# Performance work log

Measured on AMD Instinct MI355X. Metric: run time of the kernel, lower is better.

Reference implementation:

```python
import jax, jax.numpy as jnp
from jax import lax
import numpy as np

N, C_IN, C_OUT, H, W, DS = 32, 16, 1, 128, 128, 5
NC = C_OUT * C_IN  # channels fed to DUBlock convs (= out_nc*nc_d[0])


def autocorr(x, ds):
    """x:(N,C,H,W) -> xtx_raw:(N,C,C,2ds-1,2ds-1).
    xtx_raw[n,i,j,u,v] = sum_{h,w} x[n,i,h,w] * xpad[n,j,u+h,v+w]  (zero pad ds-1),
    matching torch cal_xtx (sample-wise conv3d of x with itself)."""
    n, c, h, w = x.shape
    p = ds - 1
    xp = jnp.pad(x, ((0, 0), (0, 0), (p, p), (p, p)))
    rows = []
    for u in range(2 * ds - 1):
        cols = [jnp.einsum('nihw,njhw->nij', x,
                           lax.slice(xp, (0, 0, u, v), (n, c, u + h, v + w)))
                for v in range(2 * ds - 1)]
        rows.append(jnp.stack(cols, axis=-1))
    return jnp.stack(rows, axis=-2)  # (N,C,C,K,K), K=2ds-1


def crosscorr(x, y, ds):
    """x:(N,Ci,H,W), y:(N,Co,H,W) -> xty:(N,Co,Ci,ds,ds)  (torch cal_xty, pad=(ds-1)//2)."""
    n, c, h, w = x.shape
    p = (ds - 1) // 2
    xp = jnp.pad(x, ((0, 0), (0, 0), (p, p), (p, p)))
    rows = []
    for u in range(ds):
        cols = [jnp.einsum('nohw,njhw->noj', y,
                           lax.slice(xp, (0, 0, u, v), (n, c, u + h, v + w)))
                for v in range(ds)]
        rows.append(jnp.stack(cols, axis=-1))
    return jnp.stack(rows, axis=-2)  # (N,Co,Ci,ds,ds)


def assemble_Q(R, ds):
    """Block-Toeplitz assembly. Equivalent to torch's unfold + flip + index permutation:
    Q[n,(i,p,q),(j,oi,oj)] = R[n,i,j, ds-1+oi-p, ds-1+oj-q]."""
    n, c = R.shape[0], R.shape[1]
    r = jnp.arange(ds)
    idx = (ds - 1) + r[None, :] - r[:, None]  # idx[p,o] = ds-1+o-p in [0, 2ds-2]
    Q6 = R[:, :, :, idx[:, None, :, None], idx[None, :, None, :]]  # (N,i,j,p,q,oi,oj)
    return jnp.transpose(Q6, (0, 1, 3, 4, 2, 5, 6)).reshape(n, c * ds * ds, c * ds * ds)


def dsb(x, d, y, alpha, reg):
    """DSBlock: regularized normal equations + batched SPD solve.
    x:(N,Ci,H,W), d:(N,Co,Ci,ds,ds), y:(N,Co,H,W), alpha:(N,1,1,1), reg:(1,)"""
    n, ci, h, w = x.shape
    co, ds = d.shape[1], d.shape[-1]
    Q = assemble_Q(autocorr(x, ds), ds)                               # (N, ci*ds^2, ci*ds^2)
    P = crosscorr(x, y, ds).reshape(n, co, -1).transpose(0, 2, 1)      # (N, ci*ds^2, co)
    a = alpha.reshape(n, 1, 1) * (h * w) * reg / (ds * ds * ci)        # (N,1,1)
    m = Q.shape[1]
    Q = Q + a * jnp.eye(m, dtype=Q.dtype)
    P = P + a * d.reshape(n, co, -1).transpose(0, 2, 1)
    # torch uses cholesky + cholesky_solve on SPD Q; jnp.linalg.solve computes the
    # same solution (and its vjp matches the custom CholeskySolve backward for symmetric Q).
    D = jnp.linalg.solve(Q, P)                                         # (N, ci*ds^2, co)
    return D.reshape(n, ci, ds, ds, co).transpose(0, 4, 1, 2, 3)       # (N,Co,Ci,ds,ds)


def conv3x3(x, wgt, b):
    o = lax.conv_general_dilated(x, wgt, (1, 1), ((1, 1), (1, 1)),
                                 dimension_numbers=('NCHW', 'OIHW', 'NCHW'))
    return o + b[None, :, None, None]


def dblock_fwd(x1, x2, d, y1, y2, alpha, beta, reg,
               w1, b1, w2, b2, w3, b3, w4, b4, w5, b5, w6, b6):
    d = dsb(x1, d, y1, alpha, reg)
    d = dsb(x2, d, y2, alpha, reg)
    n, co, ci, ds = d.shape[0], d.shape[1], d.shape[2], d.shape[3]
    bmap = jnp.broadcast_to(1.0 / jnp.sqrt(beta), (n, 1, ds, ds))      # (1/beta.sqrt()).repeat
    h0 = jnp.concatenate([d.reshape(n, co * ci, ds, ds), bmap], axis=1)
    # DUBlock
    t = jax.nn.relu(conv3x3(jax.nn.relu(conv3x3(h0, w1, b1)), w2, b2))
    t = jax.nn.relu(conv3x3(jax.nn.relu(conv3x3(t, w3, b3)), w4, b4))
    t = conv3x3(jax.nn.relu(conv3x3(t, w5, b5)), w6, b6) + h0[:, :-1]
    return t.reshape(n, co, ci, ds, ds)


def setup_inputs() -> dict:
    key = jax.random.key(0)
    ks = jax.random.split(key, 24)
    inp = {
        'x1': jax.random.normal(ks[0], (N, C_IN, H, W), jnp.float32),
        'x2': jax.random.normal(ks[1], (N, C_IN, H, W), jnp.float32),
        'd': jax.random.normal(ks[2], (N, C_OUT, C_IN, DS, DS), jnp.float32),
        'y1': jax.random.normal(ks[3], (N, C_OUT, H, W), jnp.float32),
        'y2': jax.random.normal(ks[4], (N, C_OUT, H, W), jnp.float32),
        'alpha': jax.random.uniform(ks[5], (N, 1, 1, 1), jnp.float32),
        'beta': jax.random.uniform(ks[6], (N, 1, 1, 1), jnp.float32),
        'reg': jnp.ones((1,), jnp.float32),
    }
    cins = [NC + 1, NC, NC, NC, NC, NC]
    for i in range(6):
        inp['w%d' % (i + 1)] = 0.05 * jax.random.normal(ks[7 + i], (NC, cins[i], 3, 3), jnp.float32)
        inp['b%d' % (i + 1)] = jnp.zeros((NC,), jnp.float32)
    return inp


def reference(x1, x2, d, y1, y2, alpha, beta, reg,
              w1, b1, w2, b2, w3, b3, w4, b4, w5, b5, w6, b6):
    return dblock_fwd(x1, x2, d, y1, y2, alpha, beta, reg,
                      w1, b1, w2, b2, w3, b3, w4, b4, w5, b5, w6, b6)
```

## Files before the change

### kernel.cpp

```cpp
#include <hip/hip_runtime.h>
#include <hip/hip_bf16.h>

constexpr int NS   = 32;
constexpr int C    = 16;
constexpr int H    = 128;
constexpr int W    = 128;
constexpr int DS   = 5;
constexpr int M    = C * DS * DS;
constexpr int NLAG = 81;

typedef short short8 __attribute__((ext_vector_type(8)));
typedef float f32x4 __attribute__((ext_vector_type(4)));

constexpr int CH_U    = 152;
constexpr int SLOT_U  = 16 * CH_U;
constexpr int SLOT_B  = SLOT_U * 2;
constexpr int RING_B  = 16 * SLOT_B;

constexpr int WREP_F  = 6 * 144 * 20 + 6 * 16;
constexpr int WREP_CH = WREP_F * 4 / 16;

constexpr int PVP = 29;

constexpr size_t RSZ  = (size_t)NS * C * C * NLAG;
constexpr int    RSZ4 = (int)(RSZ / 4);
constexpr int    CMB_BLOCKS = RSZ4 / 256;

__device__ __forceinline__ unsigned int pk_bf16(float a, float b) {
    union { __hip_bfloat162 h; unsigned int u; } cv;
    cv.h = __float22bfloat162_rn(make_float2(a, b));
    return cv.u;
}

__device__ __forceinline__ void gl_lds16(const void* g, void* l) {
    __builtin_amdgcn_global_load_lds(
        (const __attribute__((address_space(1))) unsigned int*)g,
        (__attribute__((address_space(3))) unsigned int*)l, 16, 0, 0);
}

__device__ __forceinline__ void stage4(const float* __restrict__ xn,
                                       char* sm, int row0, int tid)
{
    const int pair = tid >> 3;
    const int sub  = tid & 7;
    const int rr   = pair >> 4;
    const int ch   = pair & 15;
    const int row  = row0 + rr;
    const float4* src = (const float4*)(xn + ((size_t)ch * H + row) * W + sub * 16);
    const float4 a = src[0], b = src[1], c = src[2], d = src[3];
    unsigned short* dst = (unsigned short*)sm + (row & 15) * SLOT_U + ch * CH_U + 8 + sub * 16;
    *(uint4*)(dst)     = make_uint4(pk_bf16(a.x, a.y), pk_bf16(a.z, a.w),
                                    pk_bf16(b.x, b.y), pk_bf16(b.z, b.w));
    *(uint4*)(dst + 8) = make_uint4(pk_bf16(c.x, c.y), pk_bf16(c.z, c.w),
                                    pk_bf16(d.x, d.y), pk_bf16(d.z, d.w));
}

template<int P0, int P1>
__device__ __forceinline__ void autocorr_body(const float* __restrict__ xn,
                                              float* __restrict__ Rn,
                                              char* sm, int tid, int rbase)
{
    constexpr int U0 = P0 / 9;
    constexpr int U1 = (P1 - 1) / 9;
    constexpr int NB = U1 - U0 + 1;
    constexpr int NP = P1 - P0;
    constexpr int SLOT_Q = SLOT_B / 16;

    unsigned short* ring = (unsigned short*)sm;
    const int lane = tid & 63;
    const int wid  = tid >> 6;
    const int q    = lane >> 4;
    const int mi   = lane & 15;
    const int rh   = wid & 3;
    const int chh  = wid >> 2;

    f32x4 acc[NP];
#pragma unroll
    for (int l = 0; l < NP; ++l) acc[l] = (f32x4){0.f, 0.f, 0.f, 0.f};

    if (rbase == 0) {
        for (int f = tid; f < 4 * SLOT_Q; f += 512)
            ((uint4*)sm)[(12 + f / SLOT_Q) * SLOT_Q + (f % SLOT_Q)] = make_uint4(0, 0, 0, 0);
        if (tid < 192) {
            const int slot = tid >> 4, ch = tid & 15;
            unsigned short* sb = ring + slot * SLOT_U + ch * CH_U;
            *(uint4*)(sb)       = make_uint4(0u, 0u, 0u, 0u);
            *(uint4*)(sb + 136) = make_uint4(0u, 0u, 0u, 0u);
            *(uint4*)(sb + 144) = make_uint4(0u, 0u, 0u, 0u);
        }
        stage4(xn, sm, 0, tid);
        stage4(xn, sm, 4, tid);
    } else {
        if (tid < 256) {
            const int slot = tid >> 4, ch = tid & 15;
            unsigned short* sb = ring + slot * SLOT_U + ch * CH_U;
            *(uint4*)(sb)       = make_uint4(0u, 0u, 0u, 0u);
            *(uint4*)(sb + 136) = make_uint4(0u, 0u, 0u, 0u);
            *(uint4*)(sb + 144) = make_uint4(0u, 0u, 0u, 0u);
        }
        stage4(xn, sm, 60, tid);
        stage4(xn, sm, 64, tid);
        stage4(xn, sm, 68, tid);
    }
    __syncthreads();

    for (int s = 0; s < 64; s += 4) {
        if (s <= 52 || (s == 56 && rbase == 0)) {
            stage4(xn, sm, rbase + s + 8, tid);
        } else if (s == 56) {
            for (int f = tid; f < 4 * SLOT_Q; f += 512)
                ((uint4*)sm)[(((s + 8 + f / SLOT_Q) & 15)) * SLOT_Q + (f % SLOT_Q)] = make_uint4(0, 0, 0, 0);
        }

        const int r = s + rh;
        const unsigned short* rowA = ring + (r & 15) * SLOT_U + mi * CH_U;
#pragma unroll
        for (int cc = 0; cc < 2; ++cc) {
            const int w0 = (chh * 2 + cc) * 32;
            const uint4* pa = (const uint4*)(rowA + w0 + 8 * q);
            uint4 A0 = pa[0], A1 = pa[1], A2 = pa[2];
            unsigned int d[12] = {A0.x, A0.y, A0.z, A0.w, A1.x, A1.y, A1.z, A1.w,
                                  A2.x, A2.y, A2.z, A2.w};
            short8 bf[NB];
#pragma unroll
            for (int u = U0; u <= U1; ++u)
                bf[u - U0] = *(const short8*)(ring + ((r + u - 4 + 16) & 15) * SLOT_U +
                                              mi * CH_U + 8 + w0 + 8 * q);
#pragma unroll
            for (int v = 0; v < 9; ++v) {
                const int off = 12 - v;
                const int q4  = off >> 1;
                union { unsigned int u4[4]; short8 s8; } af;
                if (off & 1) {
#pragma unroll
                    for (int k2 = 0; k2 < 4; ++k2)
                        af.u4[k2] = (d[q4 + k2] >> 16) | (d[q4 + k2 + 1] << 16);
                } else {
#pragma unroll
                    for (int k2 = 0; k2 < 4; ++k2) af.u4[k2] = d[q4 + k2];
                }
#pragma unroll
                for (int u = U0; u <= U1; ++u) {
                    if (u * 9 + v >= P0 && u * 9 + v < P1)
                        acc[u * 9 + v - P0] = __builtin_amdgcn_mfma_f32_16x16x32_bf16(
                            af.s8, bf[u - U0], acc[u * 9 + v - P0], 0, 0, 0);
                }
            }
        }
        __syncthreads();
    }

    float* sred = (float*)sm;
    const int qr   = tid >> 4;
    const int pidx = (((qr & 3) * 4) + (qr >> 2)) * 16 + (tid & 15);
#pragma unroll
    for (int cb = 0; cb < NP; cb += 9) {
        const int nc = (NP - cb < 9) ? (NP - cb) : 9;
        __syncthreads();
#pragma unroll
        for (int pp = 0; pp < 9; ++pp) {
            if (pp < nc) {
#pragma unroll
                for (int rg = 0; rg < 4; ++rg)
                    sred[(pp * 8 + wid) * 256 + (rg * 4 + q) * 16 + mi] = acc[cb + pp][rg];
            }
        }
        __syncthreads();
        if (tid < 256) {
#pragma unroll
            for (int pp = 0; pp < 9; ++pp) {
                if (pp < nc) {
                    float ssum = 0.f;
#pragma unroll
                    for (int w8 = 0; w8 < 8; ++w8)
                        ssum += sred[(pp * 8 + w8) * 256 + pidx];
                    Rn[(size_t)tid * NLAG + P0 + cb + pp] = ssum;
                }
            }
        }
    }
}

__global__ __launch_bounds__(512, 1)
void autocorr_mfma(const float* __restrict__ x1, const float* __restrict__ x2,
                   float* __restrict__ R1a, float* __restrict__ R1b,
                   float* __restrict__ R2a, float* __restrict__ R2b)
{
    __shared__ __align__(16) char sm[RING_B];
    const int b = blockIdx.x;
    const int xcd = b & 7, k = b >> 3;
    const int sl_local = k >> 2;
    const int r2 = k & 3;
    const int half = r2 >> 1, lg = r2 & 1;
    const int slice = xcd * 8 + sl_local;
    const int n = slice & 31, zi = slice >> 5;
    const int rbase = half * 64;
    const float* xn = (zi ? x2 : x1) + (size_t)n * C * H * W;
    float* Rbase = zi ? (half ? R2b : R2a) : (half ? R1b : R1a);
    float* Rn = Rbase + (size_t)n * C * C * NLAG;
    if (lg == 0) autocorr_body< 0, 41>(xn, Rn, sm, threadIdx.x, rbase);
    else         autocorr_body<41, 81>(xn, Rn, sm, threadIdx.x, rbase);
}

__global__ __launch_bounds__(256, 1)
void mid_kernel(const float* __restrict__ x1, const float* __restrict__ x2,
                const float* __restrict__ y1, const float* __restrict__ y2,
                float* __restrict__ P1, float* __restrict__ P2,
                const float* __restrict__ w1, const float* __restrict__ b1,
                const float* __restrict__ w2, const float* __restrict__ b2,
                const float* __restrict__ w3, const float* __restrict__ b3,
                const float* __restrict__ w4, const float* __restrict__ b4,
                const float* __restrict__ w5, const float* __restrict__ b5,
                const float* __restrict__ w6, const float* __restrict__ b6,
                float* __restrict__ wrep,
                float* __restrict__ R1a, const float* __restrict__ R1b,
                float* __restrict__ R2a, const float* __restrict__ R2b)
{
    __shared__ float red[4][25];
    const int b = blockIdx.x, tid = threadIdx.x;
    if (b < 1024) {
        const int n = b & 31, j = (b >> 5) & 15, zi = b >> 9;
        const float* x = zi ? x2 : x1;
        const float* y = zi ? y2 : y1;
        float* P       = zi ? P2 : P1;

        const float* yn = y + (size_t)n * H * W;
        const float* xc = x + ((size_t)n * C + j) * H * W;

        const int wg = tid & 31, slab = tid >> 5;
        const int r0 = slab * 16;

        float acc[25];
#pragma unroll
        for (int l = 0; l < 25; ++l) acc[l] = 0.f;

        float4 yw[5];
#pragma unroll
        for (int u = 0; u < 5; ++u) {
            const int t = r0 + 1 - u;
            yw[u] = (t >= 0) ? *(const float4*)(yn + (size_t)t * W + wg * 4)
                             : make_float4(0.f, 0.f, 0.f, 0.f);
        }

#pragma unroll 4
        for (int rr = 0; rr < 16; ++rr) {
            const int r = r0 + rr;
#pragma unroll
            for (int u = 4; u >= 1; --u) yw[u] = yw[u - 1];
            const int tnew = r + 2;
            yw[0] = (tnew < H) ? *(const float4*)(yn + (size_t)tnew * W + wg * 4)
                               : make_float4(0.f, 0.f, 0.f, 0.f);

            const float* xr = xc + (size_t)r * W + wg * 4;
            float w12[12];
            float4 t4 = (wg > 0) ? *(const float4*)(xr - 4) : make_float4(0, 0, 0, 0);
            w12[0] = t4.x; w12[1] = t4.y; w12[2] = t4.z; w12[3] = t4.w;
            t4 = *(const float4*)(xr);
            w12[4] = t4.x; w12[5] = t4.y; w12[6] = t4.z; w12[7] = t4.w;
            t4 = (wg < 31) ? *(const float4*)(xr + 4) : make_float4(0, 0, 0, 0);
            w12[8] = t4.x; w12[9] = t4.y; w12[10] = t4.z; w12[11] = t4.w;

#pragma unroll
            for (int u = 0; u < 5; ++u) {
#pragma unroll
                for (int v = 0; v < 5; ++v)
                    acc[u * 5 + v] += yw[u].x * w12[2 + v] + yw[u].y * w12[3 + v] +
                                      yw[u].z * w12[4 + v] + yw[u].w * w12[5 + v];
            }
        }

        const int lane = tid & 63, wv = tid >> 6;
#pragma unroll
        for (int l = 0; l < 25; ++l) {
            float v = acc[l];
#pragma unroll
            for (int off = 32; off; off >>= 1) v += __shfl_down(v, off);
            if (lane == 0) red[wv][l] = v;
        }
        __syncthreads();
        if (tid < 25)
            P[((size_t)n * C + j) * 25 + tid] = red[0][tid] + red[1][tid] + red[2][tid] + red[3][tid];
        return;
    }
    if (b == 1024) {
        const float* wsl[6] = {w1, w2, w3, w4, w5, w6};
        const float* bsl[6] = {b1, b2, b3, b4, b5, b6};
#pragma unroll
        for (int l = 0; l < 6; ++l) {
            const int cin = (l == 0) ? 17 : 16;
            const float* ws = wsl[l];
            for (int f = tid; f < 16 * cin * 9; f += 256) {
                const int o = f / (cin * 9);
                const int rm = f - o * cin * 9;
                const int ci = rm / 9, kk = rm - ci * 9;
                wrep[l * 2880 + (o * 9 + kk) * 20 + ci] = ws[f];
            }
            if (tid < 16) wrep[17280 + l * 16 + tid] = bsl[l][tid];
        }
        return;
    }
    const int i = (b - 1025) * 256 + tid;
    if (i < RSZ4) {
        float4 a = ((float4*)R1a)[i], bb = ((const float4*)R1b)[i];
        a.x += bb.x; a.y += bb.y; a.z += bb.z; a.w += bb.w;
        ((float4*)R1a)[i] = a;
        float4 c = ((float4*)R2a)[i], d = ((const float4*)R2b)[i];
        c.x += d.x; c.y += d.y; c.z += d.z; c.w += d.w;
        ((float4*)R2a)[i] = c;
    }
}

__device__ __forceinline__ float block_sum256(float v, float* red, int t)
{
#pragma unroll
    for (int off = 32; off; off >>= 1) v += __shfl_down(v, off);
    if ((t & 63) == 0) red[t >> 6] = v;
    __syncthreads();
    float s = red[0] + red[1] + red[2] + red[3];
    __syncthreads();
    return s;
}

__device__ __forceinline__ float2 block_sum256_f2(float v0, float v1, float* red, int t)
{
#pragma unroll
    for (int off = 32; off; off >>= 1) { v0 += __shfl_down(v0, off); v1 += __shfl_down(v1, off); }
    if ((t & 63) == 0) { red[(t >> 6) * 2] = v0; red[(t >> 6) * 2 + 1] = v1; }
    __syncthreads();
    const float s0 = red[0] + red[2] + red[4] + red[6];
    const float s1 = red[1] + red[3] + red[5] + red[7];
    __syncthreads();
    return make_float2(s0, s1);
}

__device__ __forceinline__ void cg_solve(const float (&Rreg)[81],
                                         float rhs0, float rhs1,
                                         int iters, float a, int t, bool has1,
                                         float* pv, float* ap, float* red,
                                         float& z0o, float& z1o)
{
    const int jj = t & 15;
    const int e1 = t + 256;
    float z0 = 0.f, z1 = 0.f;
    float r0 = rhs0, r1 = has1 ? rhs1 : 0.f;
    float p0 = r0, p1 = r1;
    pv[(t / 25) * PVP + (t % 25)] = p0;
    if (has1) pv[(e1 / 25) * PVP + (e1 % 25)] = p1;
    float rr = block_sum256(r0 * r0 + r1 * r1, red, t);

    for (int it = 0; it < iters; ++it) {
        float pld[25], acc[25];
        const float* pj = &pv[jj * PVP];
#pragma unroll
        for (int k = 0; k < 25; ++k) pld[k] = pj[k];
#pragma unroll
        for (int k = 0; k < 25; ++k) acc[k] = 0.f;
#pragma unroll
        for (int u = 0; u < 9; ++u) {
#pragma unroll
            for (int v = 0; v < 9; ++v) {
                const float Rv = Rreg[u * 9 + v];
#pragma unroll
                for (int c = 0; c < 5; ++c) {
                    if (c < u - 4 || c > u) continue;
                    const int aa = 4 + c - u;
#pragma unroll
                    for (int dd = 0; dd < 5; ++dd) {
                        if (dd < v - 4 || dd > v) continue;
                        const int bb = 4 + dd - v;
                        acc[aa * 5 + bb] += Rv * pld[c * 5 + dd];
                    }
                }
            }
        }
#pragma unroll
        for (int k = 0; k < 25; ++k) {
            float s2 = acc[k];
            s2 += __shfl_down(s2, 8, 16);
            s2 += __shfl_down(s2, 4, 16);
            s2 += __shfl_down(s2, 2, 16);
            s2 += __shfl_down(s2, 1, 16);
            acc[k] = s2;
        }
        if (jj == 0) {
#pragma unroll
            for (int k = 0; k < 25; ++k) ap[(t >> 4) * 25 + k] = acc[k];
        }
        __syncthreads();
        const float w0 = ap[t] + a * p0;
        const float w1 = has1 ? (ap[e1] + a * p1) : 0.f;
        const float2 dots = block_sum256_f2(p0 * w0 + p1 * w1,
                                            w0 * w0 + w1 * w1, red, t);
        const float pAp = dots.x, ww = dots.y;
        const bool ok = (pAp > 1e-30f);
        const float al  = ok ? rr / pAp : 0.f;
        z0 += al * p0; z1 += al * p1;
        if (it + 1 < iters) {
            const float rrn = ok ? fmaxf(al * al * ww - rr, 0.f) : rr;
            const float be  = (rr > 1e-30f) ? rrn / rr : 0.f;
            rr = rrn;
            r0 -= al * w0; r1 -= al * w1;
            p0 = r0 + be * p0; p1 = r1 + be * p1;
            pv[(t / 25) * PVP + (t % 25)] = p0;
            if (has1) pv[(e1 / 25) * PVP + (e1 % 25)] = p1;
            __syncthreads();
        }
    }
    z0o = z0; z1o = z1;
}

__device__ __forceinline__ float conv_one(const float* __restrict__ act,
                                          const float* __restrict__ wall,
                                          int l, int idx)
{
    const int o = idx / 25, pix = idx % 25, yy = pix / 5, xx = pix % 5;
    float s = wall[17280 + l * 16 + o];
#pragma unroll
    for (int ky = 0; ky < 3; ++ky) {
        const int iy = yy + ky - 1;
        if ((unsigned)iy >= 5u) continue;
#pragma unroll
        for (int kx = 0; kx < 3; ++kx) {
            const int ix = xx + kx - 1;
            if ((unsigned)ix >= 5u) continue;
            const float* ip = act + (iy * 5 + ix) * 20;
            const float* wp = wall + l * 2880 + (o * 9 + ky * 3 + kx) * 20;
            const float4 a0 = *(const float4*)(ip);
            const float4 a1 = *(const float4*)(ip + 4);
            const float4 a2 = *(const float4*)(ip + 8);
            const float4 a3 = *(const float4*)(ip + 12);
            const float4 q0 = *(const float4*)(wp);
            const float4 q1 = *(const float4*)(wp + 4);
            const float4 q2 = *(const float4*)(wp + 8);
            const float4 q3 = *(const float4*)(wp + 12);
            s += a0.x * q0.x + a0.y * q0.y + a0.z * q0.z + a0.w * q0.w
               + a1.x * q1.x + a1.y * q1.y + a1.z * q1.z + a1.w * q1.w
               + a2.x * q2.x + a2.y * q2.y + a2.z * q2.z + a2.w * q2.w
               + a3.x * q3.x + a3.y * q3.y + a3.z * q3.z + a3.w * q3.w;
            if (l == 0) s += ip[16] * wp[16];
        }
    }
    return s;
}

__global__ __launch_bounds__(256, 1)
void solve_kernel(const float* __restrict__ R1, const float* __restrict__ R2,
                  const float* __restrict__ P1, const float* __restrict__ P2,
                  const float* __restrict__ d0, const float* __restrict__ alpha,
                  const float* __restrict__ beta, const float* __restrict__ reg,
                  const float* __restrict__ wrep,
                  float* __restrict__ out)
{
    __shared__ __align__(16) float Rl[256 * NLAG];
    __shared__ float pv[16 * PVP];
    __shared__ float ap[M];
    __shared__ float red[8];
    __shared__ float h0p[25 * 20];
    __shared__ float bufA[25 * 20], bufB[25 * 20];

    const int n = blockIdx.x, t = threadIdx.x;
    const bool has1 = (t < M - 256);
    const int e1 = t + 256;
    const float a = alpha[n] * (float)(H * W) * reg[0] / (float)(DS * DS * C);

    {
        const char* g = (const char*)(R1 + (size_t)n * 256 * NLAG);
        char* l = (char*)Rl;
        for (int f = t; f < 5184; f += 256)
            gl_lds16(g + (size_t)f * 16, l + (size_t)f * 16);
    }
    const float rhs10 = P1[(size_t)n * M + t] + a * d0[(size_t)n * M + t];
    const float rhs11 = has1 ? (P1[(size_t)n * M + e1] + a * d0[(size_t)n * M + e1]) : 0.f;
    __syncthreads();

    float Rreg[81];
    {
        const float* Rrow = &Rl[t * NLAG];
#pragma unroll
        for (int i = 0; i < 81; ++i) Rreg[i] = Rrow[i];
    }
    __syncthreads();

    {
        const char* g = (const char*)(R2 + (size_t)n * 256 * NLAG);
        char* l = (char*)Rl;
        for (int f = t; f < 5184; f += 256)
            gl_lds16(g + (size_t)f * 16, l + (size_t)f * 16);
    }
    float z1a, z1b;
    cg_solve(Rreg, rhs10, rhs11, 3, a, t, has1, pv, ap, red, z1a, z1b);
    __syncthreads();
    {
        const float* Rrow = &Rl[t * NLAG];
#pragma unroll
        for (int i = 0; i < 81; ++i) Rreg[i] = Rrow[i];
    }
    __syncthreads();

    {
        const char* g = (const char*)wrep;
        char* l = (char*)Rl;
        for (int f = t; f < WREP_CH; f += 256)
            gl_lds16(g + (size_t)f * 16, l + (size_t)f * 16);
    }
    const float rhs20 = P2[(size_t)n * M + t] + a * z1a;
    const float rhs21 = has1 ? (P2[(size_t)n * M + e1] + a * z1b) : 0.f;
    float z20, z21;
    cg_solve(Rreg, rhs20, rhs21, 7, a, t, has1, pv, ap, red, z20, z21);

    const float* wall = (const float*)Rl;
    h0p[(t % 25) * 20 + t / 25] = z20;
    if (has1) h0p[(e1 % 25) * 20 + e1 / 25] = z21;
    if (t < 25) h0p[t * 20 + 16] = rsqrtf(beta[n]);
    __syncthreads();

#pragma unroll
    for (int l = 0; l < 6; ++l) {
        const float* act = (l == 0) ? h0p : ((l & 1) ? bufA : bufB);
        float s0 = conv_one(act, wall, l, t);
        float s1 = has1 ? conv_one(act, wall, l, e1) : 0.f;
        if (l < 5) { s0 = fmaxf(s0, 0.f); s1 = fmaxf(s1, 0.f); }
        else {
            s0 += h0p[(t % 25) * 20 + t / 25];
            if (has1) s1 += h0p[(e1 % 25) * 20 + e1 / 25];
        }
        if (l == 5) {
            out[(size_t)n * M + t] = s0;
            if (has1) out[(size_t)n * M + e1] = s1;
        } else {
            float* dstb = (l & 1) ? bufB : bufA;
            dstb[(t % 25) * 20 + t / 25] = s0;
            if (has1) dstb[(e1 % 25) * 20 + e1 / 25] = s1;
        }
        __syncthreads();
    }
}

extern "C" void kernel_launch(void* const* d_in, const int* in_sizes, int n_in,
                              void* d_out, int out_size, void* d_ws, size_t ws_size,
                              hipStream_t stream)
{
    (void)in_sizes; (void)n_in; (void)out_size; (void)ws_size;
    const float* x1    = (const float*)d_in[0];
    const float* x2    = (const float*)d_in[1];
    const float* d0    = (const float*)d_in[2];
    const float* y1    = (const float*)d_in[3];
    const float* y2    = (const float*)d_in[4];
    const float* alpha = (const float*)d_in[5];
    const float* beta  = (const float*)d_in[6];
    const float* reg   = (const float*)d_in[7];
    const float* w1 = (const float*)d_in[8];  const float* b1 = (const float*)d_in[9];
    const float* w2 = (const float*)d_in[10]; const float* b2 = (const float*)d_in[11];
    const float* w3 = (const float*)d_in[12]; const float* b3 = (const float*)d_in[13];
    const float* w4 = (const float*)d_in[14]; const float* b4 = (const float*)d_in[15];
    const float* w5 = (const float*)d_in[16]; const float* b5 = (const float*)d_in[17];
    const float* w6 = (const float*)d_in[18]; const float* b6 = (const float*)d_in[19];
    float* out = (float*)d_out;

    char* wsb = (char*)d_ws;
    float* R1a = (float*)wsb;
    float* R1b = R1a + RSZ;
    float* R2a = R1b + RSZ;
    float* R2b = R2a + RSZ;
    float* P1  = R2b + RSZ;
    float* P2  = P1 + (size_t)NS * M;
    float* wrep = P2 + (size_t)NS * M;

    autocorr_mfma<<<256, 512, 0, stream>>>(x1, x2, R1a, R1b, R2a, R2b);
    mid_kernel<<<1025 + CMB_BLOCKS, 256, 0, stream>>>(x1, x2, y1, y2, P1, P2,
                                                      w1, b1, w2, b2, w3, b3,
                                                      w4, b4, w5, b5, w6, b6,
                                                      wrep, R1a, R1b, R2a, R2b);
    solve_kernel<<<NS, 256, 0, stream>>>(R1a, R2a, P1, P2, d0, alpha, beta, reg,
                                         wrep, out);
}
```

Before: 247.1 us.

## Merge autocorr, crosscorr and weight repack into one front kernel; fold R-half sum into solve

```diff
diff --git a/kernel.cpp b/kernel.cpp
--- a/kernel.cpp
+++ b/kernel.cpp
@@ -23,8 +23,6 @@
 constexpr int PVP = 29;
 
 constexpr size_t RSZ  = (size_t)NS * C * C * NLAG;
-constexpr int    RSZ4 = (int)(RSZ / 4);
-constexpr int    CMB_BLOCKS = RSZ4 / 256;
 
 __device__ __forceinline__ unsigned int pk_bf16(float a, float b) {
     union { __hip_bfloat162 h; unsigned int u; } cv;
@@ -181,132 +179,122 @@
     }
 }
 
+__device__ __forceinline__ void crosscorr_body(const float* __restrict__ yn,
+                                               const float* __restrict__ xc,
+                                               float* __restrict__ Pdst,
+                                               char* sm, int tid)
+{
+    const int wg = tid & 31, slab = tid >> 5;
+    const int r0 = slab * 8;
+
+    float4 yreg[12];
+#pragma unroll
+    for (int u = 0; u < 12; ++u) {
+        const int t_ = r0 - 2 + u;
+        yreg[u] = (t_ >= 0 && t_ < H)
+                      ? *(const float4*)(yn + (size_t)t_ * W + wg * 4)
+                      : make_float4(0.f, 0.f, 0.f, 0.f);
+    }
+
+    float acc[25];
+#pragma unroll
+    for (int l = 0; l < 25; ++l) acc[l] = 0.f;
+
+#pragma unroll
+    for (int rr = 0; rr < 8; ++rr) {
+        const int r = r0 + rr;
+        const float* xr = xc + (size_t)r * W + wg * 4;
+        float w12[12];
+        float4 t4 = (wg > 0) ? *(const float4*)(xr - 4) : make_float4(0, 0, 0, 0);
+        w12[0] = t4.x; w12[1] = t4.y; w12[2] = t4.z; w12[3] = t4.w;
+        t4 = *(const float4*)(xr);
+        w12[4] = t4.x; w12[5] = t4.y; w12[6] = t4.z; w12[7] = t4.w;
+        t4 = (wg < 31) ? *(const float4*)(xr + 4) : make_float4(0, 0, 0, 0);
+        w12[8] = t4.x; w12[9] = t4.y; w12[10] = t4.z; w12[11] = t4.w;
+
+#pragma unroll
+        for (int u = 0; u < 5; ++u) {
+            const float4 yv = yreg[rr + 4 - u];
+#pragma unroll
+            for (int v = 0; v < 5; ++v)
+                acc[u * 5 + v] += yv.x * w12[2 + v] + yv.y * w12[3 + v] +
+                                  yv.z * w12[4 + v] + yv.w * w12[5 + v];
+        }
+    }
+
+    float* red = (float*)sm;
+    const int lane = tid & 63, wv = tid >> 6;
+#pragma unroll
+    for (int l = 0; l < 25; ++l) {
+        float v = acc[l];
+#pragma unroll
+        for (int off = 32; off; off >>= 1) v += __shfl_down(v, off);
+        if (lane == 0) red[wv * 25 + l] = v;
+    }
+    __syncthreads();
+    if (tid < 25) {
+        float s = 0.f;
+#pragma unroll
+        for (int w8 = 0; w8 < 8; ++w8) s += red[w8 * 25 + tid];
+        Pdst[tid] = s;
+    }
+}
+
 __global__ __launch_bounds__(512, 1)
-void autocorr_mfma(const float* __restrict__ x1, const float* __restrict__ x2,
-                   float* __restrict__ R1a, float* __restrict__ R1b,
-                   float* __restrict__ R2a, float* __restrict__ R2b)
+void front_kernel(const float* __restrict__ x1, const float* __restrict__ x2,
+                  const float* __restrict__ y1, const float* __restrict__ y2,
+                  float* __restrict__ R1a, float* __restrict__ R1b,
+                  float* __restrict__ R2a, float* __restrict__ R2b,
+                  float* __restrict__ P1, float* __restrict__ P2,
+                  const float* __restrict__ w1, const float* __restrict__ b1,
+                  const float* __restrict__ w2, const float* __restrict__ b2,
+                  const float* __restrict__ w3, const float* __restrict__ b3,
+                  const float* __restrict__ w4, const float* __restrict__ b4,
+                  const float* __restrict__ w5, const float* __restrict__ b5,
+                  const float* __restrict__ w6, const float* __restrict__ b6,
+                  float* __restrict__ wrep)
 {
     __shared__ __align__(16) char sm[RING_B];
-    const int b = blockIdx.x;
-    const int xcd = b & 7, k = b >> 3;
-    const int sl_local = k >> 2;
-    const int r2 = k & 3;
-    const int half = r2 >> 1, lg = r2 & 1;
-    const int slice = xcd * 8 + sl_local;
-    const int n = slice & 31, zi = slice >> 5;
-    const int rbase = half * 64;
-    const float* xn = (zi ? x2 : x1) + (size_t)n * C * H * W;
-    float* Rbase = zi ? (half ? R2b : R2a) : (half ? R1b : R1a);
-    float* Rn = Rbase + (size_t)n * C * C * NLAG;
-    if (lg == 0) autocorr_body< 0, 41>(xn, Rn, sm, threadIdx.x, rbase);
-    else         autocorr_body<41, 81>(xn, Rn, sm, threadIdx.x, rbase);
-}
-
-__global__ __launch_bounds__(256, 1)
-void mid_kernel(const float* __restrict__ x1, const float* __restrict__ x2,
-                const float* __restrict__ y1, const float* __restrict__ y2,
-                float* __restrict__ P1, float* __restrict__ P2,
-                const float* __restrict__ w1, const float* __restrict__ b1,
-                const float* __restrict__ w2, const float* __restrict__ b2,
-                const float* __restrict__ w3, const float* __restrict__ b3,
-                const float* __restrict__ w4, const float* __restrict__ b4,
-                const float* __restrict__ w5, const float* __restrict__ b5,
-                const float* __restrict__ w6, const float* __restrict__ b6,
-                float* __restrict__ wrep,
-                float* __restrict__ R1a, const float* __restrict__ R1b,
-                float* __restrict__ R2a, const float* __restrict__ R2b)
-{
-    __shared__ float red[4][25];
     const int b = blockIdx.x, tid = threadIdx.x;
-    if (b < 1024) {
-        const int n = b & 31, j = (b >> 5) & 15, zi = b >> 9;
+    if (b < 256) {
+        const int xcd = b & 7, k = b >> 3;
+        const int sl_local = k >> 2;
+        const int r2 = k & 3;
+        const int half = r2 >> 1, lg = r2 & 1;
+        const int slice = xcd * 8 + sl_local;
+        const int n = slice & 31, zi = slice >> 5;
+        const int rbase = half * 64;
+        const float* xn = (zi ? x2 : x1) + (size_t)n * C * H * W;
+        float* Rbase = zi ? (half ? R2b : R2a) : (half ? R1b : R1a);
+        float* Rn = Rbase + (size_t)n * C * C * NLAG;
+        if (lg == 0) autocorr_body< 0, 41>(xn, Rn, sm, tid, rbase);
+        else         autocorr_body<41, 81>(xn, Rn, sm, tid, rbase);
+        return;
+    }
+    if (b < 1280) {
+        const int c2 = b - 256;
+        const int n = c2 & 31, j = (c2 >> 5) & 15, zi = c2 >> 9;
         const float* x = zi ? x2 : x1;
         const float* y = zi ? y2 : y1;
         float* P       = zi ? P2 : P1;
-
-        const float* yn = y + (size_t)n * H * W;
-        const float* xc = x + ((size_t)n * C + j) * H * W;
-
-        const int wg = tid & 31, slab = tid >> 5;
-        const int r0 = slab * 16;
-
-        float acc[25];
-#pragma unroll
-        for (int l = 0; l < 25; ++l) acc[l] = 0.f;
-
-        float4 yw[5];
-#pragma unroll
-        for (int u = 0; u < 5; ++u) {
-            const int t = r0 + 1 - u;
-            yw[u] = (t >= 0) ? *(const float4*)(yn + (size_t)t * W + wg * 4)
-                             : make_float4(0.f, 0.f, 0.f, 0.f);
-        }
-
-#pragma unroll 4
-        for (int rr = 0; rr < 16; ++rr) {
-            const int r = r0 + rr;
-#pragma unroll
-            for (int u = 4; u >= 1; --u) yw[u] = yw[u - 1];
-            const int tnew = r + 2;
-            yw[0] = (tnew < H) ? *(const float4*)(yn + (size_t)tnew * W + wg * 4)
-                               : make_float4(0.f, 0.f, 0.f, 0.f);
-
-            const float* xr = xc + (size_t)r * W + wg * 4;
-            float w12[12];
-            float4 t4 = (wg > 0) ? *(const float4*)(xr - 4) : make_float4(0, 0, 0, 0);
-            w12[0] = t4.x; w12[1] = t4.y; w12[2] = t4.z; w12[3] = t4.w;
-            t4 = *(const float4*)(xr);
-            w12[4] = t4.x; w12[5] = t4.y; w12[6] = t4.z; w12[7] = t4.w;
-            t4 = (wg < 31) ? *(const float4*)(xr + 4) : make_float4(0, 0, 0, 0);
-            w12[8] = t4.x; w12[9] = t4.y; w12[10] = t4.z; w12[11] = t4.w;
-
-#pragma unroll
-            for (int u = 0; u < 5; ++u) {
-#pragma unroll
-                for (int v = 0; v < 5; ++v)
-                    acc[u * 5 + v] += yw[u].x * w12[2 + v] + yw[u].y * w12[3 + v] +
-                                      yw[u].z * w12[4 + v] + yw[u].w * w12[5 + v];
-            }
-        }
-
-        const int lane = tid & 63, wv = tid >> 6;
-#pragma unroll
-        for (int l = 0; l < 25; ++l) {
-            float v = acc[l];
-#pragma unroll
-            for (int off = 32; off; off >>= 1) v += __shfl_down(v, off);
-            if (lane == 0) red[wv][l] = v;
-        }
-        __syncthreads();
-        if (tid < 25)
-            P[((size_t)n * C + j) * 25 + tid] = red[0][tid] + red[1][tid] + red[2][tid] + red[3][tid];
+        crosscorr_body(y + (size_t)n * H * W,
+                       x + ((size_t)n * C + j) * H * W,
+                       P + ((size_t)n * C + j) * 25, sm, tid);
         return;
     }
-    if (b == 1024) {
-        const float* wsl[6] = {w1, w2, w3, w4, w5, w6};
-        const float* bsl[6] = {b1, b2, b3, b4, b5, b6};
-#pragma unroll
-        for (int l = 0; l < 6; ++l) {
-            const int cin = (l == 0) ? 17 : 16;
-            const float* ws = wsl[l];
-            for (int f = tid; f < 16 * cin * 9; f += 256) {
-                const int o = f / (cin * 9);
-                const int rm = f - o * cin * 9;
-                const int ci = rm / 9, kk = rm - ci * 9;
-                wrep[l * 2880 + (o * 9 + kk) * 20 + ci] = ws[f];
-            }
-            if (tid < 16) wrep[17280 + l * 16 + tid] = bsl[l][tid];
-        }
-        return;
-    }
-    const int i = (b - 1025) * 256 + tid;
-    if (i < RSZ4) {
-        float4 a = ((float4*)R1a)[i], bb = ((const float4*)R1b)[i];
-        a.x += bb.x; a.y += bb.y; a.z += bb.z; a.w += bb.w;
-        ((float4*)R1a)[i] = a;
-        float4 c = ((float4*)R2a)[i], d = ((const float4*)R2b)[i];
-        c.x += d.x; c.y += d.y; c.z += d.z; c.w += d.w;
-        ((float4*)R2a)[i] = c;
+    const float* wsl[6] = {w1, w2, w3, w4, w5, w6};
+    const float* bsl[6] = {b1, b2, b3, b4, b5, b6};
+#pragma unroll
+    for (int l = 0; l < 6; ++l) {
+        const int cin = (l == 0) ? 17 : 16;
+        const float* ws = wsl[l];
+        for (int f = tid; f < 16 * cin * 9; f += 512) {
+            const int o = f / (cin * 9);
+            const int rm = f - o * cin * 9;
+            const int ci = rm / 9, kk = rm - ci * 9;
+            wrep[l * 2880 + (o * 9 + kk) * 20 + ci] = ws[f];
+        }
+        if (tid < 16) wrep[17280 + l * 16 + tid] = bsl[l][tid];
     }
 }
 
@@ -444,7 +432,8 @@
 }
 
 __global__ __launch_bounds__(256, 1)
-void solve_kernel(const float* __restrict__ R1, const float* __restrict__ R2,
+void solve_kernel(const float* __restrict__ R1a, const float* __restrict__ R1b,
+                  const float* __restrict__ R2a, const float* __restrict__ R2b,
                   const float* __restrict__ P1, const float* __restrict__ P2,
                   const float* __restrict__ d0, const float* __restrict__ alpha,
                   const float* __restrict__ beta, const float* __restrict__ reg,
@@ -464,7 +453,7 @@
     const float a = alpha[n] * (float)(H * W) * reg[0] / (float)(DS * DS * C);
 
     {
-        const char* g = (const char*)(R1 + (size_t)n * 256 * NLAG);
+        const char* g = (const char*)(R1a + (size_t)n * 256 * NLAG);
         char* l = (char*)Rl;
         for (int f = t; f < 5184; f += 256)
             gl_lds16(g + (size_t)f * 16, l + (size_t)f * 16);
@@ -476,13 +465,14 @@
     float Rreg[81];
     {
         const float* Rrow = &Rl[t * NLAG];
-#pragma unroll
-        for (int i = 0; i < 81; ++i) Rreg[i] = Rrow[i];
+        const float* rb   = R1b + (size_t)n * 256 * NLAG + (size_t)t * NLAG;
+#pragma unroll
+        for (int i = 0; i < 81; ++i) Rreg[i] = Rrow[i] + rb[i];
     }
     __syncthreads();
 
     {
-        const char* g = (const char*)(R2 + (size_t)n * 256 * NLAG);
+        const char* g = (const char*)(R2a + (size_t)n * 256 * NLAG);
         char* l = (char*)Rl;
         for (int f = t; f < 5184; f += 256)
             gl_lds16(g + (size_t)f * 16, l + (size_t)f * 16);
@@ -492,8 +482,9 @@
     __syncthreads();
     {
         const float* Rrow = &Rl[t * NLAG];
-#pragma unroll
-        for (int i = 0; i < 81; ++i) Rreg[i] = Rrow[i];
+        const float* rb   = R2b + (size_t)n * 256 * NLAG + (size_t)t * NLAG;
+#pragma unroll
+        for (int i = 0; i < 81; ++i) Rreg[i] = Rrow[i] + rb[i];
     }
     __syncthreads();
 
@@ -566,11 +557,10 @@
     float* P2  = P1 + (size_t)NS * M;
     float* wrep = P2 + (size_t)NS * M;
 
-    autocorr_mfma<<<256, 512, 0, stream>>>(x1, x2, R1a, R1b, R2a, R2b);
-    mid_kernel<<<1025 + CMB_BLOCKS, 256, 0, stream>>>(x1, x2, y1, y2, P1, P2,
-                                                      w1, b1, w2, b2, w3, b3,
-                                                      w4, b4, w5, b5, w6, b6,
-                                                      wrep, R1a, R1b, R2a, R2b);
-    solve_kernel<<<NS, 256, 0, stream>>>(R1a, R2a, P1, P2, d0, alpha, beta, reg,
-                                         wrep, out);
-}
+    front_kernel<<<1281, 512, 0, stream>>>(x1, x2, y1, y2,
+                                           R1a, R1b, R2a, R2b, P1, P2,
+                                           w1, b1, w2, b2, w3, b3,
+                                           w4, b4, w5, b5, w6, b6, wrep);
+    solve_kernel<<<NS, 256, 0, stream>>>(R1a, R1b, R2a, R2b, P1, P2,
+                                         d0, alpha, beta, reg, wrep, out);
+}
```

New measurement: 298.7 us. 20.9% more time.
